# Kernel tuning notes

Measured on AMD Instinct MI355X. Metric: run time of the kernel, lower is better.

Reference implementation:

```python
import jax, jax.numpy as jnp
import numpy as np

EPS = 1e-5  # BatchNorm1d default eps
NUM_HEADS = 8


def repbn(x, alpha, gamma, beta, rm, rv):
    # eval-mode RepBN over the channel (last) dim: BN(running stats) + alpha * x
    bn = (x - rm) * (gamma / jnp.sqrt(rv + EPS)) + beta
    return bn + alpha * x


def _forward(x, W_qkv, b_qkv, W_proj, b_proj, W1, b1, W2, b2, sa_w, sa_b,
             alpha1, gamma1, beta1, rm1, rv1, alpha2, gamma2, beta2, rm2, rv2):
    B, C, H, W = x.shape
    N = H * W
    D = C // NUM_HEADS
    t = x.reshape(B, C, N).transpose(0, 2, 1)  # [B, N, C]
    # --- FlashAttention (manual MHSA) ---
    qkv = (t @ W_qkv + b_qkv).reshape(B, N, 3, NUM_HEADS, D)
    q = qkv[:, :, 0].transpose(0, 2, 1, 3)  # [B, h, N, D]
    k = qkv[:, :, 1].transpose(0, 2, 1, 3)
    v = qkv[:, :, 2].transpose(0, 2, 1, 3)
    attn = jax.nn.softmax(jnp.einsum('bhnd,bhmd->bhnm', q, k) * (D ** -0.5), axis=-1)
    o = jnp.einsum('bhnm,bhmd->bhnd', attn, v).transpose(0, 2, 1, 3).reshape(B, N, C)
    o = o @ W_proj + b_proj
    # residual + blended norm (eval -> RepBN)
    t = repbn(t + o, alpha1, gamma1, beta1, rm1, rv1)
    # --- FFN with SpatialSILU activation ---
    h = t @ W1 + b1  # [B, N, cm]
    # depthwise 1x1 conv over the batch dim (channels==B per original unsqueeze(0))
    wgt = sa_w[:, None, None] * h + sa_b[:, None, None]
    h = h * jax.nn.sigmoid(wgt * h)
    f = h @ W2 + b2
    t = repbn(t + f, alpha2, gamma2, beta2, rm2, rv2)
    return t.transpose(0, 2, 1).reshape(B, C, H, W)


def setup_inputs() -> dict:
    key = jax.random.key(0)
    ks = jax.random.split(key, 8)
    B, C, H, W = 256, 256, 14, 14
    cm = 2048
    s = 0.02
    f32 = jnp.float32
    return {
        'x': jax.random.normal(ks[0], (B, C, H, W), f32),
        'W_qkv': jax.random.normal(ks[1], (C, 3 * C), f32) * s,
        'b_qkv': jnp.zeros((3 * C,), f32),
        'W_proj': jax.random.normal(ks[2], (C, C), f32) * s,
        'b_proj': jnp.zeros((C,), f32),
        'W1': jax.random.normal(ks[3], (C, cm), f32) * s,
        'b1': jnp.zeros((cm,), f32),
        'W2': jax.random.normal(ks[4], (cm, C), f32) * s,
        'b2': jnp.zeros((C,), f32),
        'sa_w': jax.random.normal(ks[5], (B,), f32) * s,
        'sa_b': jnp.zeros((B,), f32),
        'alpha1': jnp.ones((), f32),
        'gamma1': jnp.ones((C,), f32),
        'beta1': jnp.zeros((C,), f32),
        'rm1': jax.random.normal(ks[6], (C,), f32) * 0.1,
        'rv1': jnp.ones((C,), f32),
        'alpha2': jnp.ones((), f32),
        'gamma2': jnp.ones((C,), f32),
        'beta2': jnp.zeros((C,), f32),
        'rm2': jax.random.normal(ks[7], (C,), f32) * 0.1,
        'rv2': jnp.ones((C,), f32),
    }


def reference(x, W_qkv, b_qkv, W_proj, b_proj, W1, b1, W2, b2, sa_w, sa_b,
              alpha1, gamma1, beta1, rm1, rv1, alpha2, gamma2, beta2, rm2, rv2):
    return _forward(x, W_qkv, b_qkv, W_proj, b_proj, W1, b1, W2, b2, sa_w, sa_b,
                    alpha1, gamma1, beta1, rm1, rv1, alpha2, gamma2, beta2, rm2, rv2)
```

## Files before the change

### kernel.cpp

```cpp
#include <hip/hip_runtime.h>

using u16 = unsigned short;

typedef __bf16 bf16x8 __attribute__((ext_vector_type(8)));
typedef u16    u16x8  __attribute__((ext_vector_type(8)));
typedef float  f32x4  __attribute__((ext_vector_type(4)));

__device__ __forceinline__ float b2f(u16 u) {
    union { unsigned int i; float f; } c; c.i = ((unsigned int)u) << 16; return c.f;
}
__device__ __forceinline__ u16 f2b(float f) {
    union { float f; unsigned int i; } c; c.f = f;
    unsigned int i = c.i;
    return (u16)((i + 0x7FFFu + ((i >> 16) & 1u)) >> 16);
}
__device__ __forceinline__ float u2f(unsigned int u) {
    union { unsigned int i; float f; } c; c.i = u; return c.f;
}

#define AS1 __attribute__((address_space(1)))
#define AS3 __attribute__((address_space(3)))
__device__ __forceinline__ void glds16(const u16* g, u16* l) {
    __builtin_amdgcn_global_load_lds((const AS1 void*)(const void*)g,
                                     (AS3 void*)(void*)l, 16, 0, 0);
}

__global__ void btrans_f2b(const float* __restrict__ in, u16* __restrict__ out, int R, int C) {
    __shared__ u16 tile[32][33];
    const int c0 = blockIdx.x * 32, r0 = blockIdx.y * 32;
    const size_t base = (size_t)blockIdx.z * R * C;
    const int tx = threadIdx.x, ty = threadIdx.y;
    #pragma unroll
    for (int i = ty; i < 32; i += 8) {
        int r = r0 + i, c = c0 + tx;
        tile[i][tx] = (r < R && c < C) ? f2b(in[base + (size_t)r * C + c]) : (u16)0;
    }
    __syncthreads();
    #pragma unroll
    for (int i = ty; i < 32; i += 8) {
        int c = c0 + i, r = r0 + tx;
        if (c < C && r < R) out[base + (size_t)c * R + r] = tile[tx][i];
    }
}

__global__ void btrans_b2f(const u16* __restrict__ in, float* __restrict__ out, int R, int C) {
    __shared__ u16 tile[32][33];
    const int c0 = blockIdx.x * 32, r0 = blockIdx.y * 32;
    const size_t base = (size_t)blockIdx.z * R * C;
    const int tx = threadIdx.x, ty = threadIdx.y;
    #pragma unroll
    for (int i = ty; i < 32; i += 8) {
        int r = r0 + i, c = c0 + tx;
        tile[i][tx] = (r < R && c < C) ? in[base + (size_t)r * C + c] : (u16)0;
    }
    __syncthreads();
    #pragma unroll
    for (int i = ty; i < 32; i += 8) {
        int c = c0 + i, r = r0 + tx;
        if (c < C && r < R) out[base + (size_t)c * R + r] = b2f(tile[tx][i]);
    }
}

template<int EPI>
__launch_bounds__(512, 4)
__global__ void gemm_bt(const u16* __restrict__ A, const u16* __restrict__ BT,
                        const float* __restrict__ bias, u16* __restrict__ C,
                        int M, int N, int K, int row0,
                        const u16* __restrict__ R0,
                        const float* __restrict__ g, const float* __restrict__ be,
                        const float* __restrict__ rmv, const float* __restrict__ rvv,
                        const float* __restrict__ alpha,
                        const float* __restrict__ saw, const float* __restrict__ sab) {
    __shared__ __align__(16) u16 SL[24576];
    const int tid  = threadIdx.x;
    const int wave = tid >> 6, lane = tid & 63;
    const int wm = wave >> 1, wn = wave & 1;
    const int quad = lane >> 4, l16 = lane & 15;

    const unsigned gx = gridDim.x;
    unsigned lin = blockIdx.y * gx + blockIdx.x;
    const unsigned nwg = gx * gridDim.y;
    const unsigned q8 = nwg >> 3, r8 = nwg & 7;
    const unsigned xcd = lin & 7, loc = lin >> 3;
    lin = (xcd < r8 ? xcd * (q8 + 1) : r8 * (q8 + 1) + (xcd - r8) * q8) + loc;
    const int m0 = (int)(lin / gx) * 256, n0 = (int)(lin % gx) * 128;

    const int srow = lane >> 2;
    const int scol = (((lane & 3) ^ ((srow >> 1) & 3)) * 8);
    const size_t aoff0 = (size_t)(m0 + wave * 32 + srow) * K + scol;
    const size_t aoff1 = aoff0 + (size_t)16 * K;
    const size_t boff  = (size_t)(n0 + wave * 16 + srow) * K + scol;

    const int cfrag = (quad ^ ((l16 >> 1) & 3)) * 8;

    f32x4 acc[4][4] = {};
    const int niter = K >> 5;

    auto stage = [&](int buf, size_t kn) {
        glds16(A  + aoff0 + kn, SL + buf * 8192 + wave * 1024);
        glds16(A  + aoff1 + kn, SL + buf * 8192 + wave * 1024 + 512);
        glds16(BT + boff  + kn, SL + 16384 + buf * 4096 + wave * 512);
    };

    auto kstep = [&](int cur, int kt) {
        __syncthreads();
        if (kt + 1 < niter) stage(cur ^ 1, (size_t)(kt + 1) << 5);
        const u16* ab = SL + cur * 8192;
        const u16* bb = SL + 16384 + cur * 4096;
        bf16x8 af[4], bfr[4];
        #pragma unroll
        for (int i = 0; i < 4; i++)
            af[i] = *(const bf16x8*)&ab[(wm * 64 + i * 16 + l16) * 32 + cfrag];
        #pragma unroll
        for (int j = 0; j < 4; j++)
            bfr[j] = *(const bf16x8*)&bb[(wn * 64 + j * 16 + l16) * 32 + cfrag];
        #pragma unroll
        for (int i = 0; i < 4; i++)
            #pragma unroll
            for (int j = 0; j < 4; j++)
                acc[i][j] = __builtin_amdgcn_mfma_f32_16x16x32_bf16(af[i], bfr[j], acc[i][j], 0, 0, 0);
    };

    stage(0, 0);
    int kt = 0;
    for (; kt + 2 <= niter; kt += 2) { kstep(0, kt); kstep(1, kt + 1); }
    if (kt < niter) kstep(kt & 1, kt);

    __syncthreads();

    float alphav = 0.f;
    if (EPI == 1) alphav = alpha[0];

    float biasv[4], k0v[4], k1v[4];
    #pragma unroll
    for (int j = 0; j < 4; j++) {
        const int col = n0 + wn * 64 + j * 16 + l16;
        biasv[j] = bias[col];
        if (EPI == 1) {
            float sc = g[col] * rsqrtf(rvv[col] + 1e-5f);
            k1v[j] = sc + alphav;
            k0v[j] = be[col] - rmv[col] * sc;
        }
    }

    const int dup = l16 & 1;
    const int pr  = l16 >> 1;
    u16* Crow = C + (size_t)(m0 + wm * 64 + quad * 4 + 2 * dup) * N
                  + (n0 + wn * 64 + pr * 2);

    auto emit = [&]() {
        #pragma unroll
        for (int i = 0; i < 4; i++) {
            float swv4[4], sbv4[4];
            if (EPI == 2) {
                #pragma unroll
                for (int r = 0; r < 4; r++) {
                    const int row = row0 + m0 + wm * 64 + i * 16 + quad * 4 + r;
                    const int bidx = row / 196;
                    swv4[r] = saw[bidx]; sbv4[r] = sab[bidx];
                }
            }
            #pragma unroll
            for (int j = 0; j < 4; j++) {
                float vv[4];
                #pragma unroll
                for (int r = 0; r < 4; r++) {
                    float v = acc[i][j][r] + biasv[j];
                    if (EPI == 1) {
                        const int rowL = (wm & 1) * 64 + i * 16 + quad * 4 + r;
                        const int colp = wn * 64 + j * 16 + (l16 & ~1);
                        unsigned rd = *(const unsigned*)&SL[rowL * 128 + colp];
                        unsigned fb = dup ? (rd & 0xffff0000u) : (rd << 16);
                        float x = v + u2f(fb);
                        v = fmaf(x, k1v[j], k0v[j]);
                    } else if (EPI == 2) {
                        float w = fmaf(swv4[r], v, sbv4[r]);
                        v = v / (1.f + __expf(-w * v));
                    }
                    vv[r] = v;
                }
                unsigned D[4];
                #pragma unroll
                for (int r = 0; r < 4; r++) {
                    float o  = __shfl_xor(vv[r], 1, 64);
                    float lo = dup ? o : vv[r];
                    float hi = dup ? vv[r] : o;
                    unsigned d;
                    asm("v_cvt_pk_bf16_f32 %0, %1, %2" : "=v"(d) : "v"(lo), "v"(hi));
                    D[r] = d;
                }
                unsigned s0 = dup ? D[2] : D[0];
                unsigned s1 = dup ? D[3] : D[1];
                u16* p = Crow + (size_t)i * 16 * N + j * 16;
                *(unsigned*)p       = s0;
                *(unsigned*)(p + N) = s1;
            }
        }
    };

    if (EPI == 1) {
        #pragma unroll
        for (int h = 0; h < 2; h++) {
            for (int c = tid; c < 2048; c += 512) {
                int row = c >> 4, colc = (c & 15) * 8;
                *(u16x8*)&SL[row * 128 + colc] =
                    *(const u16x8*)&R0[(size_t)(m0 + h * 128 + row) * N + n0 + colc];
            }
            __syncthreads();
            if ((wm >> 1) == h) emit();
            __syncthreads();
        }
    } else {
        emit();
    }
}

__launch_bounds__(256)
__global__ void attn_kernel(const u16* __restrict__ qkv, u16* __restrict__ o) {
    __shared__ __align__(16) u16 Kb[224 * 32];
    __shared__ __align__(16) u16 Vt[32 * 232];
    __shared__ __align__(16) u16 Pl[4][16 * 232];
    const int tid  = threadIdx.x;
    const int wave = tid >> 6, lane = tid & 63;
    const int quad = lane >> 4, l16 = lane & 15;
    const int b = blockIdx.x >> 3, h = blockIdx.x & 7;
    const u16* qg = qkv + (size_t)b * 196 * 768 + h * 32;
    const float scale = 0.17677669529663687f;

    for (int idx = tid; idx < 896; idx += 256) {
        int row = idx >> 2, dp = (idx & 3) * 8;
        u16x8 kv = {};
        if (row < 196) kv = *(const u16x8*)&qg[(size_t)row * 768 + 256 + dp];
        *(u16x8*)&Kb[row * 32 + dp] = kv;
    }
    for (int idx = tid; idx < 224 * 32; idx += 256) {
        int row = idx >> 5, d = idx & 31;
        Vt[d * 232 + row] = (row < 196) ? qg[(size_t)row * 768 + 512 + d] : (u16)0;
    }
    for (int c = lane; c < 16 * 24; c += 64) {
        int m = c / 24, cc = 208 + (c % 24);
        Pl[wave][m * 232 + cc] = 0;
    }
    __syncthreads();

    for (int t = wave; t < 13; t += 4) {
        const int m0 = t * 16;
        bf16x8 aq = {};
        const int qrow = m0 + l16;
        if (qrow < 196) aq = *(const bf16x8*)&qg[(size_t)qrow * 768 + quad * 8];

        f32x4 s[13];
        #pragma unroll
        for (int ct = 0; ct < 13; ct++) {
            bf16x8 bk = *(const bf16x8*)&Kb[(ct * 16 + l16) * 32 + quad * 8];
            s[ct] = __builtin_amdgcn_mfma_f32_16x16x32_bf16(aq, bk, (f32x4){0.f, 0.f, 0.f, 0.f}, 0, 0, 0);
        }
        if (l16 >= 4) {
            #pragma unroll
            for (int r = 0; r < 4; r++) s[12][r] = -1e30f;
        }
        float mx[4] = {-1e30f, -1e30f, -1e30f, -1e30f};
        #pragma unroll
        for (int ct = 0; ct < 13; ct++)
            #pragma unroll
            for (int r = 0; r < 4; r++) mx[r] = fmaxf(mx[r], s[ct][r]);
        #pragma unroll
        for (int off = 1; off < 16; off <<= 1)
            #pragma unroll
            for (int r = 0; r < 4; r++) mx[r] = fmaxf(mx[r], __shfl_xor(mx[r], off, 64));
        float sum[4] = {0.f, 0.f, 0.f, 0.f};
        #pragma unroll
        for (int ct = 0; ct < 13; ct++) {
            #pragma unroll
            for (int r = 0; r < 4; r++) {
                float p = __expf((s[ct][r] - mx[r]) * scale);
                sum[r] += p;
                Pl[wave][(quad * 4 + r) * 232 + ct * 16 + l16] = f2b(p);
            }
        }
        #pragma unroll
        for (int off = 1; off < 16; off <<= 1)
            #pragma unroll
            for (int r = 0; r < 4; r++) sum[r] += __shfl_xor(sum[r], off, 64);
        float inv[4];
        #pragma unroll
        for (int r = 0; r < 4; r++) inv[r] = 1.f / sum[r];

        #pragma unroll
        for (int nt = 0; nt < 2; nt++) {
            f32x4 ao = {0.f, 0.f, 0.f, 0.f};
            #pragma unroll
            for (int kc = 0; kc < 7; kc++) {
                bf16x8 ap = *(const bf16x8*)&Pl[wave][l16 * 232 + kc * 32 + quad * 8];
                bf16x8 bv = *(const bf16x8*)&Vt[(nt * 16 + l16) * 232 + kc * 32 + quad * 8];
                ao = __builtin_amdgcn_mfma_f32_16x16x32_bf16(ap, bv, ao, 0, 0, 0);
            }
            #pragma unroll
            for (int r = 0; r < 4; r++) {
                const int gm = m0 + quad * 4 + r;
                if (gm < 196)
                    o[((size_t)b * 196 + gm) * 256 + h * 32 + nt * 16 + l16] = f2b(ao[r] * inv[r]);
            }
        }
    }
}

extern "C" void kernel_launch(void* const* d_in, const int* in_sizes, int n_in,
                              void* d_out, int out_size, void* d_ws, size_t ws_size,
                              hipStream_t stream) {
    const float* x      = (const float*)d_in[0];
    const float* Wqkv   = (const float*)d_in[1];
    const float* bqkv   = (const float*)d_in[2];
    const float* Wproj  = (const float*)d_in[3];
    const float* bproj  = (const float*)d_in[4];
    const float* W1     = (const float*)d_in[5];
    const float* b1     = (const float*)d_in[6];
    const float* W2     = (const float*)d_in[7];
    const float* b2     = (const float*)d_in[8];
    const float* saw    = (const float*)d_in[9];
    const float* sab    = (const float*)d_in[10];
    const float* alpha1 = (const float*)d_in[11];
    const float* g1     = (const float*)d_in[12];
    const float* be1    = (const float*)d_in[13];
    const float* rm1    = (const float*)d_in[14];
    const float* rv1    = (const float*)d_in[15];
    const float* alpha2 = (const float*)d_in[16];
    const float* g2     = (const float*)d_in[17];
    const float* be2    = (const float*)d_in[18];
    const float* rm2    = (const float*)d_in[19];
    const float* rv2    = (const float*)d_in[20];

    const int B = 256, Cc = 256, Np = 196, CM = 2048;
    const int M = B * Np;

    auto al = [](size_t s) { return (s + 255) & ~(size_t)255; };
    char* ws = (char*)d_ws;
    const size_t o_t0  = 0;
    const size_t o_t1  = o_t0 + al((size_t)M * Cc * 2);
    const size_t o_wq  = o_t1 + al((size_t)M * Cc * 2);
    const size_t o_wp  = o_wq + al((size_t)768 * Cc * 2);
    const size_t o_w1  = o_wp + al((size_t)Cc * Cc * 2);
    const size_t o_w2  = o_w1 + al((size_t)Cc * CM * 2);
    const size_t o_scr = o_w2 + al((size_t)CM * Cc * 2);
    const size_t S = (ws_size > o_scr) ? ws_size - o_scr : 0;

    u16* t0     = (u16*)(ws + o_t0);
    u16* t1b    = (u16*)(ws + o_t1);
    u16* WqkvT  = (u16*)(ws + o_wq);
    u16* WprojT = (u16*)(ws + o_wp);
    u16* W1T    = (u16*)(ws + o_w1);
    u16* W2T    = (u16*)(ws + o_w2);
    u16* scr    = (u16*)(ws + o_scr);
    u16* t2     = t0;
    u16* obuf   = (u16*)d_out;
    float* out  = (float*)d_out;

    int nq = 1; while (nq < 4 && ((size_t)(M / nq) * 768 * 2) > S) nq *= 2;
    const int nf_opts[6] = {1, 2, 4, 14, 28, 56};
    int nf = 56;
    for (int i = 0; i < 6; ++i) {
        if (((size_t)(M / nf_opts[i]) * CM * 2) <= S) { nf = nf_opts[i]; break; }
    }
    const int Mq = M / nq, Bq = B / nq;
    const int Mf = M / nf;

    dim3 tb(32, 8, 1);
    btrans_f2b<<<dim3((Np + 31) / 32, (Cc + 31) / 32, B), tb, 0, stream>>>(x, t0, Cc, Np);
    btrans_f2b<<<dim3(768 / 32, Cc / 32, 1), tb, 0, stream>>>(Wqkv,  WqkvT,  Cc, 768);
    btrans_f2b<<<dim3(Cc  / 32, Cc / 32, 1), tb, 0, stream>>>(Wproj, WprojT, Cc, Cc);
    btrans_f2b<<<dim3(CM  / 32, Cc / 32, 1), tb, 0, stream>>>(W1,    W1T,    Cc, CM);
    btrans_f2b<<<dim3(Cc  / 32, CM / 32, 1), tb, 0, stream>>>(W2,    W2T,    CM, Cc);

    for (int c = 0; c < nq; ++c) {
        gemm_bt<0><<<dim3(768 / 128, Mq / 256), 512, 0, stream>>>(
            t0 + (size_t)c * Mq * Cc, WqkvT, bqkv, scr, Mq, 768, Cc, 0,
            nullptr, nullptr, nullptr, nullptr, nullptr, nullptr, nullptr, nullptr);
        attn_kernel<<<dim3(Bq * 8), 256, 0, stream>>>(scr, obuf + (size_t)c * Mq * Cc);
    }

    gemm_bt<1><<<dim3(Cc / 128, M / 256), 512, 0, stream>>>(
        obuf, WprojT, bproj, t1b, M, Cc, Cc, 0,
        t0, g1, be1, rm1, rv1, alpha1, nullptr, nullptr);

    for (int c = 0; c < nf; ++c) {
        gemm_bt<2><<<dim3(CM / 128, Mf / 256), 512, 0, stream>>>(
            t1b + (size_t)c * Mf * Cc, W1T, b1, scr, Mf, CM, Cc, c * Mf,
            nullptr, nullptr, nullptr, nullptr, nullptr, nullptr, saw, sab);
        gemm_bt<1><<<dim3(Cc / 128, Mf / 256), 512, 0, stream>>>(
            scr, W2T, b2, t2 + (size_t)c * Mf * Cc, Mf, Cc, CM, 0,
            t1b + (size_t)c * Mf * Cc, g2, be2, rm2, rv2, alpha2, nullptr, nullptr);
    }

    btrans_b2f<<<dim3((Cc + 31) / 32, (Np + 31) / 32, B), tb, 0, stream>>>(t2, out, Np, Cc);
}
```

Before: 526.2 us.

## Add persistent K=256 GEMM keeping weight tile in registers with double-buffered A

Adds a gemm_bres kernel for the K=256 GEMMs (QKV, proj, FFN up). Each block keeps its 128-column B slice in registers for the whole K and loops persistently over 64-row A tiles. The A tiles are double-buffered into LDS with async global_load_lds, and block IDs are remapped for XCD locality. This is meant to cut repeated weight loads and improve load/compute overlap. It costs more register pressure, the grid size is capped, and the proj epilogue now reads the residual directly from global memory.

```diff
diff --git a/kernel.cpp b/kernel.cpp
--- a/kernel.cpp
+++ b/kernel.cpp
@@ -14,8 +14,10 @@
     unsigned int i = c.i;
     return (u16)((i + 0x7FFFu + ((i >> 16) & 1u)) >> 16);
 }
-__device__ __forceinline__ float u2f(unsigned int u) {
-    union { unsigned int i; float f; } c; c.i = u; return c.f;
+__device__ __forceinline__ unsigned cvtpk(float lo, float hi) {
+    unsigned d;
+    asm("v_cvt_pk_bf16_f32 %0, %1, %2" : "=v"(d) : "v"(lo), "v"(hi));
+    return d;
 }
 
 #define AS1 __attribute__((address_space(1)))
@@ -58,6 +60,155 @@
     for (int i = ty; i < 32; i += 8) {
         int c = c0 + i, r = r0 + tx;
         if (c < C && r < R) out[base + (size_t)c * R + r] = b2f(tile[tx][i]);
+    }
+}
+
+template<int EPI>
+__launch_bounds__(512, 4)
+__global__ void gemm_bres(const u16* __restrict__ A, const u16* __restrict__ BT,
+                          const float* __restrict__ bias, u16* __restrict__ C,
+                          int N, int H, int row0,
+                          const u16* __restrict__ R0,
+                          const float* __restrict__ g, const float* __restrict__ be,
+                          const float* __restrict__ rmv, const float* __restrict__ rvv,
+                          const float* __restrict__ alpha,
+                          const float* __restrict__ saw, const float* __restrict__ sab) {
+    __shared__ __align__(16) u16 SL[2][16384];
+    const int tid = threadIdx.x, wave = tid >> 6, lane = tid & 63;
+    const int wm = wave >> 2, wn = wave & 3;
+    const int quad = lane >> 4, l16 = lane & 15;
+    const int G = gridDim.y;
+
+    const unsigned gx = gridDim.x;
+    unsigned lin = blockIdx.y * gx + blockIdx.x;
+    const unsigned nwg = gx * (unsigned)G;
+    const unsigned q8 = nwg >> 3, r8 = nwg & 7;
+    const unsigned xcd = lin & 7, loc = lin >> 3;
+    lin = (xcd < r8 ? xcd * (q8 + 1) : r8 * (q8 + 1) + (xcd - r8) * q8) + loc;
+    const int n0 = (int)(lin % gx) * 128;
+    const int by = (int)(lin / gx);
+    if (by >= H) return;
+
+    bf16x8 bfr[2][8];
+    #pragma unroll
+    for (int j = 0; j < 2; j++) {
+        const size_t rb = (size_t)(n0 + wn * 32 + j * 16 + l16) * 256 + quad * 8;
+        #pragma unroll
+        for (int kt = 0; kt < 8; kt++)
+            bfr[j][kt] = *(const bf16x8*)&BT[rb + kt * 32];
+    }
+
+    int gOff[4], dOff[4];
+    #pragma unroll
+    for (int t = 0; t < 4; t++) {
+        const int rl = wave * 8 + t * 2 + (lane >> 5);
+        const int sl = (lane & 31) ^ (rl & 7);
+        gOff[t] = rl * 256 + sl * 8;
+        dOff[t] = (wave * 8 + t * 2) * 256;
+    }
+
+    auto stageA = [&](int buf, int hh) {
+        const u16* src = A + (size_t)hh * 16384;
+        u16* dst = &SL[buf][0];
+        #pragma unroll
+        for (int t = 0; t < 4; t++)
+            glds16(src + gOff[t], dst + dOff[t]);
+    };
+
+    const int rA0 = wm * 32 + l16;
+    const int aB0 = rA0 * 256, aB1 = aB0 + 16 * 256;
+    const int keyA = l16 & 7;
+
+    const int dup = l16 & 1, pr = l16 >> 1;
+    const float alphav = (EPI == 1) ? alpha[0] : 0.f;
+    float biasv[2], k0p[2][2], k1p[2][2];
+    #pragma unroll
+    for (int j = 0; j < 2; j++) {
+        biasv[j] = bias[n0 + wn * 32 + j * 16 + l16];
+        if (EPI == 1) {
+            #pragma unroll
+            for (int p = 0; p < 2; p++) {
+                const int col = n0 + wn * 32 + j * 16 + pr * 2 + p;
+                const float sc = g[col] * rsqrtf(rvv[col] + 1e-5f);
+                k1p[j][p] = sc + alphav;
+                k0p[j][p] = be[col] - rmv[col] * sc;
+            }
+        }
+    }
+
+    stageA(0, by);
+    int cur = 0;
+    for (int hi = by; hi < H; hi += G) {
+        if (hi == by)       { asm volatile("s_waitcnt vmcnt(0)"  ::: "memory"); }
+        else if (EPI == 1)  { asm volatile("s_waitcnt vmcnt(16)" ::: "memory"); }
+        else                { asm volatile("s_waitcnt vmcnt(8)"  ::: "memory"); }
+        __builtin_amdgcn_s_barrier();
+        __builtin_amdgcn_sched_barrier(0);
+        const int nxt = cur ^ 1;
+        if (hi + G < H) stageA(nxt, hi + G);
+
+        const u16* Ab = &SL[cur][0];
+        f32x4 acc[2][2] = {};
+        #pragma unroll
+        for (int kt = 0; kt < 8; kt++) {
+            const int sw = (((kt * 4 + quad) ^ keyA)) * 8;
+            bf16x8 a0 = *(const bf16x8*)&Ab[aB0 + sw];
+            bf16x8 a1 = *(const bf16x8*)&Ab[aB1 + sw];
+            acc[0][0] = __builtin_amdgcn_mfma_f32_16x16x32_bf16(a0, bfr[0][kt], acc[0][0], 0, 0, 0);
+            acc[0][1] = __builtin_amdgcn_mfma_f32_16x16x32_bf16(a0, bfr[1][kt], acc[0][1], 0, 0, 0);
+            acc[1][0] = __builtin_amdgcn_mfma_f32_16x16x32_bf16(a1, bfr[0][kt], acc[1][0], 0, 0, 0);
+            acc[1][1] = __builtin_amdgcn_mfma_f32_16x16x32_bf16(a1, bfr[1][kt], acc[1][1], 0, 0, 0);
+        }
+
+        const int m0h = hi * 64;
+        u16* Crow = C + (size_t)(m0h + wm * 32 + quad * 4 + 2 * dup) * N
+                      + (n0 + wn * 32 + pr * 2);
+        const int r0i = 2 * dup, r1i = r0i + 1;
+
+        #pragma unroll
+        for (int i = 0; i < 2; i++) {
+            float swv4[4], sbv4[4];
+            if (EPI == 2) {
+                #pragma unroll
+                for (int r = 0; r < 4; r++) {
+                    const int rg = row0 + m0h + wm * 32 + i * 16 + quad * 4 + r;
+                    const int bidx = rg / 196;
+                    swv4[r] = saw[bidx]; sbv4[r] = sab[bidx];
+                }
+            }
+            #pragma unroll
+            for (int j = 0; j < 2; j++) {
+                float vv[4];
+                #pragma unroll
+                for (int r = 0; r < 4; r++) {
+                    float v = acc[i][j][r] + biasv[j];
+                    if (EPI == 2) {
+                        const float w = fmaf(swv4[r], v, sbv4[r]);
+                        v = v / (1.f + __expf(-w * v));
+                    }
+                    vv[r] = v;
+                }
+                float ot[4];
+                #pragma unroll
+                for (int r = 0; r < 4; r++) ot[r] = __shfl_xor(vv[r], 1, 64);
+                float lo0 = dup ? ot[r0i] : vv[r0i], hi0 = dup ? vv[r0i] : ot[r0i];
+                float lo1 = dup ? ot[r1i] : vv[r1i], hi1 = dup ? vv[r1i] : ot[r1i];
+                if (EPI == 1) {
+                    const u16* rp = R0 + (size_t)(m0h + wm * 32 + i * 16 + quad * 4 + r0i) * N
+                                       + (n0 + wn * 32 + j * 16 + pr * 2);
+                    const unsigned rd0 = *(const unsigned*)rp;
+                    const unsigned rd1 = *(const unsigned*)(rp + N);
+                    lo0 = fmaf(lo0 + b2f((u16)(rd0 & 0xffff)), k1p[j][0], k0p[j][0]);
+                    hi0 = fmaf(hi0 + b2f((u16)(rd0 >> 16)),    k1p[j][1], k0p[j][1]);
+                    lo1 = fmaf(lo1 + b2f((u16)(rd1 & 0xffff)), k1p[j][0], k0p[j][0]);
+                    hi1 = fmaf(hi1 + b2f((u16)(rd1 >> 16)),    k1p[j][1], k0p[j][1]);
+                }
+                u16* p = Crow + (size_t)i * 16 * N + j * 16;
+                *(unsigned*)p       = cvtpk(lo0, hi0);
+                *(unsigned*)(p + N) = cvtpk(lo1, hi1);
+            }
+        }
+        cur = nxt;
     }
 }
 
@@ -171,7 +322,8 @@
                         const int colp = wn * 64 + j * 16 + (l16 & ~1);
                         unsigned rd = *(const unsigned*)&SL[rowL * 128 + colp];
                         unsigned fb = dup ? (rd & 0xffff0000u) : (rd << 16);
-                        float x = v + u2f(fb);
+                        union { unsigned u; float f; } cc; cc.u = fb;
+                        float x = v + cc.f;
                         v = fmaf(x, k1v[j], k0v[j]);
                     } else if (EPI == 2) {
                         float w = fmaf(swv4[r], v, sbv4[r]);
@@ -185,9 +337,7 @@
                     float o  = __shfl_xor(vv[r], 1, 64);
                     float lo = dup ? o : vv[r];
                     float hi = dup ? vv[r] : o;
-                    unsigned d;
-                    asm("v_cvt_pk_bf16_f32 %0, %1, %2" : "=v"(d) : "v"(lo), "v"(hi));
-                    D[r] = d;
+                    D[r] = cvtpk(lo, hi);
                 }
                 unsigned s0 = dup ? D[2] : D[0];
                 unsigned s1 = dup ? D[3] : D[1];
@@ -372,19 +522,27 @@
     btrans_f2b<<<dim3(Cc  / 32, CM / 32, 1), tb, 0, stream>>>(W2,    W2T,    CM, Cc);
 
     for (int c = 0; c < nq; ++c) {
-        gemm_bt<0><<<dim3(768 / 128, Mq / 256), 512, 0, stream>>>(
-            t0 + (size_t)c * Mq * Cc, WqkvT, bqkv, scr, Mq, 768, Cc, 0,
+        const int Hq = Mq / 64;
+        const int Gq = (Hq < 98) ? Hq : 98;
+        gemm_bres<0><<<dim3(768 / 128, Gq), 512, 0, stream>>>(
+            t0 + (size_t)c * Mq * Cc, WqkvT, bqkv, scr, 768, Hq, 0,
             nullptr, nullptr, nullptr, nullptr, nullptr, nullptr, nullptr, nullptr);
         attn_kernel<<<dim3(Bq * 8), 256, 0, stream>>>(scr, obuf + (size_t)c * Mq * Cc);
     }
 
-    gemm_bt<1><<<dim3(Cc / 128, M / 256), 512, 0, stream>>>(
-        obuf, WprojT, bproj, t1b, M, Cc, Cc, 0,
-        t0, g1, be1, rm1, rv1, alpha1, nullptr, nullptr);
+    {
+        const int Hp = M / 64;
+        const int Gp = (Hp < 392) ? Hp : 392;
+        gemm_bres<1><<<dim3(Cc / 128, Gp), 512, 0, stream>>>(
+            obuf, WprojT, bproj, t1b, Cc, Hp, 0,
+            t0, g1, be1, rm1, rv1, alpha1, nullptr, nullptr);
+    }
 
     for (int c = 0; c < nf; ++c) {
-        gemm_bt<2><<<dim3(CM / 128, Mf / 256), 512, 0, stream>>>(
-            t1b + (size_t)c * Mf * Cc, W1T, b1, scr, Mf, CM, Cc, c * Mf,
+        const int Hf = Mf / 64;
+        const int Gf = (Hf < 49) ? Hf : 49;
+        gemm_bres<2><<<dim3(CM / 128, Gf), 512, 0, stream>>>(
+            t1b + (size_t)c * Mf * Cc, W1T, b1, scr, CM, Hf, c * Mf,
             nullptr, nullptr, nullptr, nullptr, nullptr, nullptr, saw, sab);
         gemm_bt<1><<<dim3(Cc / 128, Mf / 256), 512, 0, stream>>>(
             scr, W2T, b2, t2 + (size_t)c * Mf * Cc, Mf, Cc, CM, 0,
```

Measured after the change: 782.5 us. 1.49x slower.
